# Performance work log

Measured on AMD Instinct MI355X. Metric: run time of the kernel, lower is better.

Reference implementation:

```python
import jax, jax.numpy as jnp
import numpy as np

N = 50000   # nodes
E = 512000  # edges
D = 64      # embedding_dim
L = 4       # num_layers
ATOM_DIMS = np.array([119, 5, 12, 12, 10, 6, 6, 2, 2])  # OGB atom feature vocab sizes
BOND_DIMS = np.array([5, 6, 2])                          # OGB bond feature vocab sizes


def _ln(x, g, b, eps=1e-5):
    m = x.mean(-1, keepdims=True)
    v = x.var(-1, keepdims=True)
    return (x - m) * jax.lax.rsqrt(v + eps) * g + b


def setup_inputs() -> dict:
    key = jax.random.key(0)
    ks = jax.random.split(key, 12)
    s = 0.05
    x = jax.random.randint(ks[0], (N, 9), 0, jnp.asarray(ATOM_DIMS)[None, :])
    edge_attr = jax.random.randint(ks[1], (E, 3), 0, jnp.asarray(BOND_DIMS)[None, :])
    edge_index = jax.random.randint(ks[2], (2, E), 0, N)
    # padded embedding tables: [n_feats, max_vocab, D]
    atom_emb = jax.random.normal(ks[3], (9, 119, D), jnp.float32) * s
    bond_emb = jax.random.normal(ks[4], (3, 6, D), jnp.float32) * s
    eps = jnp.zeros((L,), jnp.float32)  # GIN eps, init 0
    W1 = jax.random.normal(ks[5], (L, D, 2 * D), jnp.float32) * s
    b1 = jnp.zeros((L, 2 * D), jnp.float32)
    W2 = jax.random.normal(ks[6], (L, 2 * D, D), jnp.float32) * s
    b2 = jnp.zeros((L, D), jnp.float32)
    ln_g = jnp.ones((L, D), jnp.float32)
    ln_b = jnp.zeros((L, D), jnp.float32)
    Wu1 = jax.random.normal(ks[7], (L, 3 * D, 3 * D), jnp.float32) * s
    bu1 = jnp.zeros((L, 3 * D), jnp.float32)
    ug = jnp.ones((L, 3 * D), jnp.float32)
    ub = jnp.zeros((L, 3 * D), jnp.float32)
    Wu2 = jax.random.normal(ks[8], (L, 3 * D, D), jnp.float32) * s
    bu2 = jnp.zeros((L, D), jnp.float32)
    return dict(x=x, edge_attr=edge_attr, edge_index=edge_index,
                atom_emb=atom_emb, bond_emb=bond_emb, eps=eps,
                W1=W1, b1=b1, W2=W2, b2=b2, ln_g=ln_g, ln_b=ln_b,
                Wu1=Wu1, bu1=bu1, ug=ug, ub=ub, Wu2=Wu2, bu2=bu2)


def reference(x, edge_attr, edge_index, atom_emb, bond_emb, eps,
              W1, b1, W2, b2, ln_g, ln_b, Wu1, bu1, ug, ub, Wu2, bu2):
    # Atom/Bond encoders: sum of per-column categorical embeddings
    node = atom_emb[jnp.arange(9)[None, :], x].sum(axis=1)       # [N, D]
    edge = bond_emb[jnp.arange(3)[None, :], edge_attr].sum(axis=1)  # [E, D]
    src, dst = edge_index[0], edge_index[1]
    for l in range(L):
        # MyGINConv (GINE): aggregate relu(x_src + e) at dst, mlp((1+eps)x + agg)
        msg = jax.nn.relu(node[src] + edge)                      # [E, D]
        agg = jax.ops.segment_sum(msg, dst, num_segments=N)      # [N, D]
        h = (1.0 + eps[l]) * node + agg
        h = jax.nn.relu(h @ W1[l] + b1[l]) @ W2[l] + b2[l]       # conv MLP
        h = _ln(h, ln_g[l], ln_b[l])                             # batch_norms[l] (LayerNorm)
        node = jax.nn.relu(h) + node                             # dropout=identity (eval) + residual
        # SparseEdgeUpdateLayer (residual=True)
        cat = jnp.concatenate([node[src], node[dst], edge], axis=-1)  # [E, 3D]
        m = _ln(cat @ Wu1[l] + bu1[l], ug[l], ub[l])
        edge = jax.nn.relu(m) @ Wu2[l] + bu2[l] + edge
    return node, edge
```

## Files before the change

kernel.cpp:

```cpp
#include <hip/hip_runtime.h>
#include <hip/hip_bf16.h>


#define GIN_N 50000
#define GIN_E 512000

typedef __attribute__((ext_vector_type(8))) short short8;
typedef __attribute__((ext_vector_type(4))) float f32x4;
typedef unsigned short u16;

__device__ __forceinline__ u16 bf16r(float x) {
    unsigned u = __builtin_bit_cast(unsigned, x);
    u += 0x7fffu + ((u >> 16) & 1u);
    return (u16)(u >> 16);
}
__device__ __forceinline__ float bf16f(u16 h) {
    unsigned u = ((unsigned)h) << 16;
    return __builtin_bit_cast(float, u);
}

__global__ __launch_bounds__(256) void zero_f32(float* __restrict__ p, int n) {
    int i = blockIdx.x * 256 + threadIdx.x;
    if (i < n) p[i] = 0.f;
}
__global__ __launch_bounds__(256) void zero_i32(int* __restrict__ p, int n) {
    int i = blockIdx.x * 256 + threadIdx.x;
    if (i < n) p[i] = 0;
}

__global__ __launch_bounds__(256) void atom_encode(const int* __restrict__ x,
        const float* __restrict__ emb, float* __restrict__ node, int N) {
    int idx = blockIdx.x * 256 + threadIdx.x;
    int n = idx >> 6, lane = idx & 63;
    if (n >= N) return;
    float s = 0.f;
#pragma unroll
    for (int f = 0; f < 9; ++f) {
        int v = x[n * 9 + f];
        s += emb[(f * 119 + v) * 64 + lane];
    }
    node[(size_t)n * 64 + lane] = s;
}

__global__ __launch_bounds__(256) void csr_hist(const int* __restrict__ dst,
                                                int* __restrict__ deg, int E) {
    int e = blockIdx.x * 256 + threadIdx.x;
    if (e < E) atomicAdd(&deg[dst[e]], 1);
}
__global__ __launch_bounds__(256) void csr_scan(const int* __restrict__ deg,
                                                int* __restrict__ cursor, int N) {
    __shared__ int ps[256];
    const int t = threadIdx.x;
    const int chunk = (N + 255) / 256;
    const int base = t * chunk;
    int s = 0;
    for (int i = 0; i < chunk; ++i) {
        int idx = base + i;
        if (idx < N) s += deg[idx];
    }
    ps[t] = s;
    __syncthreads();
    for (int off = 1; off < 256; off <<= 1) {
        int v = (t >= off) ? ps[t - off] : 0;
        __syncthreads();
        ps[t] += v;
        __syncthreads();
    }
    int run = ps[t] - s;
    for (int i = 0; i < chunk; ++i) {
        int idx = base + i;
        if (idx < N) { cursor[idx] = run; run += deg[idx]; }
    }
}
__global__ __launch_bounds__(256) void csr_fill(const int* __restrict__ dst,
        int* __restrict__ cursor, int* __restrict__ perm, int E) {
    int e = blockIdx.x * 256 + threadIdx.x;
    if (e < E) {
        int d = dst[e];
        int pos = atomicAdd(&cursor[d], 1);
        perm[pos] = e;
    }
}
__global__ __launch_bounds__(256) void permute_ei(const int* __restrict__ src,
        const int* __restrict__ dst, const int* __restrict__ perm,
        int* __restrict__ srcS, int* __restrict__ dstS, int E) {
    int i = blockIdx.x * 256 + threadIdx.x;
    if (i < E) {
        int pe = perm[i];
        srcS[i] = src[pe];
        dstS[i] = dst[pe];
    }
}

__global__ __launch_bounds__(256) void bond_encode_scatter(
        const int* __restrict__ ea, const float* __restrict__ emb,
        u16* __restrict__ edgeB, const int* __restrict__ perm,
        const int* __restrict__ srcS, const int* __restrict__ dstS,
        const float* __restrict__ node, float* __restrict__ agg, int E) {
    int idx = blockIdx.x * 256 + threadIdx.x;
    int e = idx >> 6, lane = idx & 63;
    if (e >= E) return;
    int pe = perm[e];
    float s = 0.f;
#pragma unroll
    for (int f = 0; f < 3; ++f) {
        int v = ea[pe * 3 + f];
        s += emb[(f * 6 + v) * 64 + lane];
    }
    edgeB[(size_t)e * 64 + lane] = bf16r(s);
    int si = srcS[e], di = dstS[e];
    float msg = fmaxf(node[(size_t)si * 64 + lane] + s, 0.f);
    unsafeAtomicAdd(&agg[(size_t)di * 64 + lane], msg);
}

__global__ __launch_bounds__(256) void pack_b1(const float* __restrict__ W,
        u16* __restrict__ out, int K, int Nc, int F) {
    int tid = blockIdx.x * 256 + threadIdx.x;
    int lane = tid & 63;
    int frag = (tid >> 6) % F;
    int layer = tid / (F * 64);
    int tpr = Nc / 16;
    int ks = frag / tpr, tt = frag % tpr;
    int k0 = ks * 32 + ((lane >> 4) << 3);
    int col = tt * 16 + (lane & 15);
    const float* w = W + (size_t)layer * K * Nc;
    u16* o = out + ((size_t)layer * F + frag) * 512 + (size_t)lane * 8;
#pragma unroll
    for (int j = 0; j < 8; ++j) o[j] = bf16r(w[(size_t)(k0 + j) * Nc + col]);
}
__global__ __launch_bounds__(256) void pack_b2(const float* __restrict__ W,
        u16* __restrict__ out, int K, int Nc, int F) {
    int tid = blockIdx.x * 256 + threadIdx.x;
    int lane = tid & 63;
    int frag = (tid >> 6) % F;
    int layer = tid / (F * 64);
    int tpr = Nc / 16;
    int ks = frag / tpr, tt = frag % tpr;
    int k0 = ks * 32 + ((lane >> 4) << 3);
    int col = tt * 16 + (lane & 15);
    const float* w = W + (size_t)layer * K * Nc;
    u16* o = out + ((size_t)layer * F + frag) * 1024 + (size_t)lane * 8;
#pragma unroll
    for (int j = 0; j < 8; ++j) {
        float v = w[(size_t)(k0 + j) * Nc + col];
        u16 hi = bf16r(v);
        o[j] = hi;
        o[512 + j] = bf16r(v - bf16f(hi));
    }
}

__global__ __launch_bounds__(256, 2) void node_mlp(
        float* __restrict__ node, u16* __restrict__ nodeB,
        float* __restrict__ agg,
        const float* __restrict__ epsArr, int l,
        const u16* __restrict__ pw1, const u16* __restrict__ pw2,
        const float* __restrict__ b1, const float* __restrict__ b2,
        const float* __restrict__ lng, const float* __restrict__ lnb, int N) {
    __shared__ u16 xH[64][72], xL[64][72];
    __shared__ u16 hH[64][136], hL[64][136];
    __shared__ float pS[4][64], pS2[4][64], lnM[64], lnR[64];
    const int t = threadIdx.x, w = t >> 6, lane = t & 63;
    const int g = lane >> 4, c0 = lane & 15;
    const float epf = 1.f + epsArr[l];

#pragma unroll
    for (int i = 0; i < 16; ++i) {
        int r = w * 16 + i;
        int n = blockIdx.x * 64 + r;
        float x = 0.f;
        if (n < N) {
            size_t o = (size_t)n * 64 + lane;
            x = epf * node[o] + agg[o];
            agg[o] = 0.f;
        }
        u16 h = bf16r(x);
        xH[r][lane] = h;
        xL[r][lane] = bf16r(x - bf16f(h));
    }
    __syncthreads();

    f32x4 a1[4][2];
#pragma unroll
    for (int sp = 0; sp < 4; ++sp)
#pragma unroll
        for (int lt = 0; lt < 2; ++lt) a1[sp][lt] = (f32x4)0.f;
#pragma unroll
    for (int ks = 0; ks < 2; ++ks) {
        short8 aH[4], aL[4];
#pragma unroll
        for (int sp = 0; sp < 4; ++sp) {
            aH[sp] = *(const short8*)&xH[sp * 16 + c0][ks * 32 + g * 8];
            aL[sp] = *(const short8*)&xL[sp * 16 + c0][ks * 32 + g * 8];
        }
#pragma unroll
        for (int lt = 0; lt < 2; ++lt) {
            const u16* p = pw1 + (size_t)(ks * 8 + w * 2 + lt) * 1024 + (size_t)lane * 8;
            short8 bH = *(const short8*)p;
            short8 bL = *(const short8*)(p + 512);
#pragma unroll
            for (int sp = 0; sp < 4; ++sp) {
                a1[sp][lt] = __builtin_amdgcn_mfma_f32_16x16x32_bf16(aH[sp], bH, a1[sp][lt], 0, 0, 0);
                a1[sp][lt] = __builtin_amdgcn_mfma_f32_16x16x32_bf16(aH[sp], bL, a1[sp][lt], 0, 0, 0);
                a1[sp][lt] = __builtin_amdgcn_mfma_f32_16x16x32_bf16(aL[sp], bH, a1[sp][lt], 0, 0, 0);
            }
        }
    }
#pragma unroll
    for (int lt = 0; lt < 2; ++lt) {
        int col = w * 32 + lt * 16 + c0;
        float bias = b1[col];
#pragma unroll
        for (int sp = 0; sp < 4; ++sp)
#pragma unroll
            for (int rg = 0; rg < 4; ++rg) {
                int r = sp * 16 + g * 4 + rg;
                float v = fmaxf(a1[sp][lt][rg] + bias, 0.f);
                u16 h = bf16r(v);
                hH[r][col] = h;
                hL[r][col] = bf16r(v - bf16f(h));
            }
    }
    __syncthreads();

    f32x4 a2[4];
#pragma unroll
    for (int sp = 0; sp < 4; ++sp) a2[sp] = (f32x4)0.f;
#pragma unroll
    for (int ks = 0; ks < 4; ++ks) {
        const u16* p = pw2 + (size_t)(ks * 4 + w) * 1024 + (size_t)lane * 8;
        short8 bH = *(const short8*)p;
        short8 bL = *(const short8*)(p + 512);
#pragma unroll
        for (int sp = 0; sp < 4; ++sp) {
            short8 aH = *(const short8*)&hH[sp * 16 + c0][ks * 32 + g * 8];
            short8 aL = *(const short8*)&hL[sp * 16 + c0][ks * 32 + g * 8];
            a2[sp] = __builtin_amdgcn_mfma_f32_16x16x32_bf16(aH, bH, a2[sp], 0, 0, 0);
            a2[sp] = __builtin_amdgcn_mfma_f32_16x16x32_bf16(aH, bL, a2[sp], 0, 0, 0);
            a2[sp] = __builtin_amdgcn_mfma_f32_16x16x32_bf16(aL, bH, a2[sp], 0, 0, 0);
        }
    }
    float bias2 = b2[w * 16 + c0];
    float s1v[4][4], s2v[4][4];
#pragma unroll
    for (int sp = 0; sp < 4; ++sp)
#pragma unroll
        for (int rg = 0; rg < 4; ++rg) {
            float v = a2[sp][rg] + bias2;
            a2[sp][rg] = v;
            s1v[sp][rg] = v;
            s2v[sp][rg] = v * v;
        }
#pragma unroll
    for (int off = 1; off < 16; off <<= 1)
#pragma unroll
        for (int sp = 0; sp < 4; ++sp)
#pragma unroll
            for (int rg = 0; rg < 4; ++rg) {
                s1v[sp][rg] += __shfl_xor(s1v[sp][rg], off);
                s2v[sp][rg] += __shfl_xor(s2v[sp][rg], off);
            }
    if (c0 == 0) {
#pragma unroll
        for (int sp = 0; sp < 4; ++sp)
#pragma unroll
            for (int rg = 0; rg < 4; ++rg) {
                int r = sp * 16 + g * 4 + rg;
                pS[w][r] = s1v[sp][rg];
                pS2[w][r] = s2v[sp][rg];
            }
    }
    __syncthreads();
    if (t < 64) {
        float a = pS[0][t] + pS[1][t] + pS[2][t] + pS[3][t];
        float b = pS2[0][t] + pS2[1][t] + pS2[2][t] + pS2[3][t];
        float mean = a * (1.f / 64.f);
        float var = b * (1.f / 64.f) - mean * mean;
        lnM[t] = mean;
        lnR[t] = rsqrtf(var + 1e-5f);
    }
    __syncthreads();

    int col = w * 16 + c0;
    float gg = lng[col], bc = lnb[col];
#pragma unroll
    for (int sp = 0; sp < 4; ++sp)
#pragma unroll
        for (int rg = 0; rg < 4; ++rg) {
            int r = sp * 16 + g * 4 + rg;
            int n = blockIdx.x * 64 + r;
            if (n < N) {
                size_t o = (size_t)n * 64 + col;
                float y = (a2[sp][rg] - lnM[r]) * lnR[r] * gg + bc;
                float out = fmaxf(y, 0.f) + node[o];
                node[o] = out;
                nodeB[o] = bf16r(out);
            }
        }
}

template <bool SCATTER>
__global__ __launch_bounds__(256, 4) void edge_update_v7(
        const int* __restrict__ src, const int* __restrict__ dst,
        const int* __restrict__ perm,
        const float* __restrict__ node, const u16* __restrict__ nodeB,
        u16* __restrict__ edgeB, float* __restrict__ edgeF,
        float* __restrict__ agg,
        const u16* __restrict__ pb1, const u16* __restrict__ pb2,
        const float* __restrict__ bu1, const float* __restrict__ ug,
        const float* __restrict__ ub, const float* __restrict__ bu2) {
    __shared__ u16 cat[64][202];
    __shared__ u16 eold[64][66];
    __shared__ float pS[4][64], pS2[4][64];
    __shared__ float lnM[64], lnR[64];
    __shared__ int dstL[64], srcL[64];
    const int t = threadIdx.x, w = t >> 6, lane = t & 63;
    const int g = lane >> 4, c0 = lane & 15;
    const int tile = (blockIdx.x & 7) * (gridDim.x >> 3) + (blockIdx.x >> 3);
    const long eB = (long)tile * 64;

    if (t < 64) { dstL[t] = dst[eB + t]; srcL[t] = src[eB + t]; }
#pragma unroll
    for (int i = 0; i < 16; ++i) {
        int r = w * 16 + i;
        long ge = eB + r;
        int s = src[ge], d = dst[ge];
        cat[r][lane]       = nodeB[(size_t)s * 64 + lane];
        cat[r][64 + lane]  = nodeB[(size_t)d * 64 + lane];
        u16 ev = edgeB[(size_t)ge * 64 + lane];
        cat[r][128 + lane] = ev;
        eold[r][lane] = ev;
    }
    __syncthreads();

    f32x4 acc[4][3];
#pragma unroll
    for (int sp = 0; sp < 4; ++sp)
#pragma unroll
        for (int lt = 0; lt < 3; ++lt) acc[sp][lt] = (f32x4)0.f;
#pragma unroll
    for (int ks = 0; ks < 6; ++ks) {
        short8 a[4];
#pragma unroll
        for (int sp = 0; sp < 4; ++sp)
            a[sp] = *(const short8*)&cat[sp * 16 + c0][ks * 32 + g * 8];
#pragma unroll
        for (int lt = 0; lt < 3; ++lt) {
            const u16* p = pb1 + (size_t)(ks * 12 + w * 3 + lt) * 512 + (size_t)lane * 8;
            short8 b = *(const short8*)p;
#pragma unroll
            for (int sp = 0; sp < 4; ++sp)
                acc[sp][lt] = __builtin_amdgcn_mfma_f32_16x16x32_bf16(a[sp], b, acc[sp][lt], 0, 0, 0);
        }
    }

    float bs[3];
#pragma unroll
    for (int lt = 0; lt < 3; ++lt) bs[lt] = bu1[w * 48 + lt * 16 + c0];
    float s1v[4][4], s2v[4][4];
#pragma unroll
    for (int sp = 0; sp < 4; ++sp)
#pragma unroll
        for (int rg = 0; rg < 4; ++rg) { s1v[sp][rg] = 0.f; s2v[sp][rg] = 0.f; }
#pragma unroll
    for (int sp = 0; sp < 4; ++sp)
#pragma unroll
        for (int lt = 0; lt < 3; ++lt)
#pragma unroll
            for (int rg = 0; rg < 4; ++rg) {
                float v = acc[sp][lt][rg] + bs[lt];
                acc[sp][lt][rg] = v;
                s1v[sp][rg] += v;
                s2v[sp][rg] += v * v;
            }
#pragma unroll
    for (int off = 1; off < 16; off <<= 1)
#pragma unroll
        for (int sp = 0; sp < 4; ++sp)
#pragma unroll
            for (int rg = 0; rg < 4; ++rg) {
                s1v[sp][rg] += __shfl_xor(s1v[sp][rg], off);
                s2v[sp][rg] += __shfl_xor(s2v[sp][rg], off);
            }
    if (c0 == 0) {
#pragma unroll
        for (int sp = 0; sp < 4; ++sp)
#pragma unroll
            for (int rg = 0; rg < 4; ++rg) {
                int r = sp * 16 + g * 4 + rg;
                pS[w][r] = s1v[sp][rg];
                pS2[w][r] = s2v[sp][rg];
            }
    }
    __syncthreads();
    if (t < 64) {
        float a = pS[0][t] + pS[1][t] + pS[2][t] + pS[3][t];
        float b = pS2[0][t] + pS2[1][t] + pS2[2][t] + pS2[3][t];
        float mean = a * (1.f / 192.f);
        float var = b * (1.f / 192.f) - mean * mean;
        lnM[t] = mean;
        lnR[t] = rsqrtf(var + 1e-5f);
    }
    __syncthreads();

#pragma unroll
    for (int lt = 0; lt < 3; ++lt) {
        int col = w * 48 + lt * 16 + c0;
        float gg = ug[col], bb = ub[col];
#pragma unroll
        for (int sp = 0; sp < 4; ++sp)
#pragma unroll
            for (int rg = 0; rg < 4; ++rg) {
                int r = sp * 16 + g * 4 + rg;
                float v = (acc[sp][lt][rg] - lnM[r]) * lnR[r] * gg + bb;
                cat[r][col] = bf16r(fmaxf(v, 0.f));
            }
    }
    __syncthreads();

    f32x4 a2[4];
#pragma unroll
    for (int sp = 0; sp < 4; ++sp) a2[sp] = (f32x4)0.f;
#pragma unroll
    for (int ks = 0; ks < 6; ++ks) {
        const u16* p = pb2 + (size_t)(ks * 4 + w) * 512 + (size_t)lane * 8;
        short8 b = *(const short8*)p;
#pragma unroll
        for (int sp = 0; sp < 4; ++sp) {
            short8 a = *(const short8*)&cat[sp * 16 + c0][ks * 32 + g * 8];
            a2[sp] = __builtin_amdgcn_mfma_f32_16x16x32_bf16(a, b, a2[sp], 0, 0, 0);
        }
    }
    __syncthreads();

    float* msgF = (float*)&cat[0][0];
    const int col = w * 16 + c0;
    const float bb2 = bu2[col];
#pragma unroll
    for (int sp = 0; sp < 4; ++sp)
#pragma unroll
        for (int rg = 0; rg < 4; ++rg) {
            int r = sp * 16 + g * 4 + rg;
            long ge = eB + r;
            float eNew = a2[sp][rg] + bb2 + bf16f(eold[r][col]);
            if (SCATTER) {
                edgeB[(size_t)ge * 64 + col] = bf16r(eNew);
                float msg = fmaxf(node[(size_t)srcL[r] * 64 + col] + eNew, 0.f);
                msgF[r * 66 + col] = msg;
            } else {
                edgeF[(size_t)perm[ge] * 64 + col] = eNew;
            }
        }

    if (SCATTER) {
        __syncthreads();
        const int colR = t & 63;
        const int h = t >> 6;
        float accm = 0.f;
#pragma unroll 1
        for (int r = h * 16; r < h * 16 + 16; ++r) {
            accm += msgF[r * 66 + colR];
            bool flush = (r == h * 16 + 15) || (dstL[r + 1] != dstL[r]);
            if (flush) {
                unsafeAtomicAdd(&agg[(size_t)dstL[r] * 64 + colR], accm);
                accm = 0.f;
            }
        }
    }
}

extern "C" void kernel_launch(void* const* d_in, const int* in_sizes, int n_in,
                              void* d_out, int out_size, void* d_ws, size_t ws_size,
                              hipStream_t stream) {
    const int*   x         = (const int*)d_in[0];
    const int*   edge_attr = (const int*)d_in[1];
    const int*   edge_index= (const int*)d_in[2];
    const float* atom_emb  = (const float*)d_in[3];
    const float* bond_emb  = (const float*)d_in[4];
    const float* eps       = (const float*)d_in[5];
    const float* W1        = (const float*)d_in[6];
    const float* b1        = (const float*)d_in[7];
    const float* W2        = (const float*)d_in[8];
    const float* b2        = (const float*)d_in[9];
    const float* ln_g      = (const float*)d_in[10];
    const float* ln_b      = (const float*)d_in[11];
    const float* Wu1       = (const float*)d_in[12];
    const float* bu1       = (const float*)d_in[13];
    const float* ug        = (const float*)d_in[14];
    const float* ub        = (const float*)d_in[15];
    const float* Wu2       = (const float*)d_in[16];
    const float* bu2       = (const float*)d_in[17];

    const int N = GIN_N, E = GIN_E;
    const int* src = edge_index;
    const int* dst = edge_index + E;

    float* node  = (float*)d_out;
    float* edgeF = (float*)d_out + (size_t)N * 64;

    char* ws = (char*)d_ws;
    float* agg   = (float*)ws;  ws += (size_t)N * 64 * 4;
    u16*   nodeB = (u16*)ws;    ws += (size_t)N * 64 * 2;
    u16*   edgeB = (u16*)ws;    ws += (size_t)E * 64 * 2;
    int*   perm  = (int*)ws;    ws += (size_t)E * 4;
    int*   srcS  = (int*)ws;    ws += (size_t)E * 4;
    int*   dstS  = (int*)ws;    ws += (size_t)E * 4;
    int*   deg   = (int*)ws;    ws += (size_t)N * 4;
    int*   cursor= (int*)ws;    ws += (size_t)(N + 1) * 4;
    u16* pb1     = (u16*)ws;    ws += (size_t)4 * 72 * 512 * 2;
    u16* pb2     = (u16*)ws;    ws += (size_t)4 * 24 * 512 * 2;
    u16* pw1     = (u16*)ws;    ws += (size_t)4 * 16 * 1024 * 2;
    u16* pw2     = (u16*)ws;    ws += (size_t)4 * 16 * 1024 * 2;

    pack_b1<<<(4 * 72 * 64) / 256, 256, 0, stream>>>(Wu1, pb1, 192, 192, 72);
    pack_b1<<<(4 * 24 * 64) / 256, 256, 0, stream>>>(Wu2, pb2, 192, 64, 24);
    pack_b2<<<(4 * 16 * 64) / 256, 256, 0, stream>>>(W1, pw1, 64, 128, 16);
    pack_b2<<<(4 * 16 * 64) / 256, 256, 0, stream>>>(W2, pw2, 128, 64, 16);

    zero_i32<<<(N + 255) / 256, 256, 0, stream>>>(deg, N);
    csr_hist<<<E / 256, 256, 0, stream>>>(dst, deg, E);
    csr_scan<<<1, 256, 0, stream>>>(deg, cursor, N);
    csr_fill<<<E / 256, 256, 0, stream>>>(dst, cursor, perm, E);
    permute_ei<<<E / 256, 256, 0, stream>>>(src, dst, perm, srcS, dstS, E);

    atom_encode<<<(N * 64 + 255) / 256, 256, 0, stream>>>(x, atom_emb, node, N);
    zero_f32<<<(N * 64) / 256, 256, 0, stream>>>(agg, N * 64);
    bond_encode_scatter<<<(E * 64) / 256, 256, 0, stream>>>(edge_attr, bond_emb,
        edgeB, perm, srcS, dstS, node, agg, E);

    const int nodeBlocks = (N + 63) / 64;
    for (int l = 0; l < 4; ++l) {
        node_mlp<<<nodeBlocks, 256, 0, stream>>>(node, nodeB, agg, eps, l,
            pw1 + (size_t)l * 16 * 1024, pw2 + (size_t)l * 16 * 1024,
            b1 + (size_t)l * 128, b2 + (size_t)l * 64,
            ln_g + (size_t)l * 64, ln_b + (size_t)l * 64, N);
        if (l < 3)
            edge_update_v7<true><<<E / 64, 256, 0, stream>>>(srcS, dstS, perm,
                node, nodeB, edgeB, edgeF, agg,
                pb1 + (size_t)l * 72 * 512, pb2 + (size_t)l * 24 * 512,
                bu1 + (size_t)l * 192,
                ug + (size_t)l * 192, ub + (size_t)l * 192,
                bu2 + (size_t)l * 64);
        else
            edge_update_v7<false><<<E / 64, 256, 0, stream>>>(srcS, dstS, perm,
                node, nodeB, edgeB, edgeF, agg,
                pb1 + (size_t)l * 72 * 512, pb2 + (size_t)l * 24 * 512,
                bu1 + (size_t)l * 192,
                ug + (size_t)l * 192, ub + (size_t)l * 192,
                bu2 + (size_t)l * 64);
    }
}
```

Baseline: 1.016 ms.

## Segment-reduce bond scatter, vectorize edge tile loads, drop eold LDS, widen scan

The initial bond-encode scatter now stages messages for a 64-edge tile in shared memory. It then does a segmented reduction over dst-sorted edges before the atomics, which cuts the number of atomic adds. The edge update kernel loads the edge tile with 8-byte vector loads, keeps the old edge values in registers instead of a separate LDS array, and raises the occupancy hint to 5 blocks per CU. The CSR scan uses 1024 threads. Together these aim to reduce atomic traffic and LDS use, with some added register pressure.

Result: slower. 1.243 ms (+22.3%).

```diff
diff --git a/kernel.cpp b/kernel.cpp
--- a/kernel.cpp
+++ b/kernel.cpp
@@ -6,6 +6,7 @@
 #define GIN_E 512000
 
 typedef __attribute__((ext_vector_type(8))) short short8;
+typedef __attribute__((ext_vector_type(4))) short short4v;
 typedef __attribute__((ext_vector_type(4))) float f32x4;
 typedef unsigned short u16;
 
@@ -47,11 +48,11 @@
     int e = blockIdx.x * 256 + threadIdx.x;
     if (e < E) atomicAdd(&deg[dst[e]], 1);
 }
-__global__ __launch_bounds__(256) void csr_scan(const int* __restrict__ deg,
-                                                int* __restrict__ cursor, int N) {
-    __shared__ int ps[256];
+__global__ __launch_bounds__(1024) void csr_scan(const int* __restrict__ deg,
+                                                 int* __restrict__ cursor, int N) {
+    __shared__ int ps[1024];
     const int t = threadIdx.x;
-    const int chunk = (N + 255) / 256;
+    const int chunk = (N + 1023) / 1024;
     const int base = t * chunk;
     int s = 0;
     for (int i = 0; i < chunk; ++i) {
@@ -60,7 +61,7 @@
     }
     ps[t] = s;
     __syncthreads();
-    for (int off = 1; off < 256; off <<= 1) {
+    for (int off = 1; off < 1024; off <<= 1) {
         int v = (t >= off) ? ps[t - off] : 0;
         __syncthreads();
         ps[t] += v;
@@ -92,25 +93,45 @@
     }
 }
 
-__global__ __launch_bounds__(256) void bond_encode_scatter(
+__global__ __launch_bounds__(256) void bond_encode_seg(
         const int* __restrict__ ea, const float* __restrict__ emb,
         u16* __restrict__ edgeB, const int* __restrict__ perm,
         const int* __restrict__ srcS, const int* __restrict__ dstS,
-        const float* __restrict__ node, float* __restrict__ agg, int E) {
-    int idx = blockIdx.x * 256 + threadIdx.x;
-    int e = idx >> 6, lane = idx & 63;
-    if (e >= E) return;
-    int pe = perm[e];
-    float s = 0.f;
-#pragma unroll
-    for (int f = 0; f < 3; ++f) {
-        int v = ea[pe * 3 + f];
-        s += emb[(f * 6 + v) * 64 + lane];
-    }
-    edgeB[(size_t)e * 64 + lane] = bf16r(s);
-    int si = srcS[e], di = dstS[e];
-    float msg = fmaxf(node[(size_t)si * 64 + lane] + s, 0.f);
-    unsafeAtomicAdd(&agg[(size_t)di * 64 + lane], msg);
+        const float* __restrict__ node, float* __restrict__ agg) {
+    __shared__ float msgF[64][66];
+    __shared__ int dstL[64];
+    const int t = threadIdx.x, w = t >> 6, lane = t & 63;
+    const int tile = (blockIdx.x & 7) * (gridDim.x >> 3) + (blockIdx.x >> 3);
+    const long eB = (long)tile * 64;
+
+    if (t < 64) dstL[t] = dstS[eB + t];
+#pragma unroll 1
+    for (int i = 0; i < 16; ++i) {
+        int r = w * 16 + i;
+        long e = eB + r;
+        int pe = perm[e];
+        float s = 0.f;
+#pragma unroll
+        for (int f = 0; f < 3; ++f) {
+            int v = ea[pe * 3 + f];
+            s += emb[(f * 6 + v) * 64 + lane];
+        }
+        edgeB[(size_t)e * 64 + lane] = bf16r(s);
+        int si = srcS[e];
+        msgF[r][lane] = fmaxf(node[(size_t)si * 64 + lane] + s, 0.f);
+    }
+    __syncthreads();
+    const int colR = t & 63;
+    const int h = t >> 6;
+    float acc = 0.f;
+#pragma unroll 1
+    for (int r = h * 16; r < h * 16 + 16; ++r) {
+        acc += msgF[r][colR];
+        if (r == h * 16 + 15 || dstL[r + 1] != dstL[r]) {
+            unsafeAtomicAdd(&agg[(size_t)dstL[r] * 64 + colR], acc);
+            acc = 0.f;
+        }
+    }
 }
 
 __global__ __launch_bounds__(256) void pack_b1(const float* __restrict__ W,
@@ -299,7 +320,7 @@
 }
 
 template <bool SCATTER>
-__global__ __launch_bounds__(256, 4) void edge_update_v7(
+__global__ __launch_bounds__(256, 5) void edge_update_v8(
         const int* __restrict__ src, const int* __restrict__ dst,
         const int* __restrict__ perm,
         const float* __restrict__ node, const u16* __restrict__ nodeB,
@@ -309,7 +330,6 @@
         const float* __restrict__ bu1, const float* __restrict__ ug,
         const float* __restrict__ ub, const float* __restrict__ bu2) {
     __shared__ u16 cat[64][202];
-    __shared__ u16 eold[64][66];
     __shared__ float pS[4][64], pS2[4][64];
     __shared__ float lnM[64], lnR[64];
     __shared__ int dstL[64], srcL[64];
@@ -324,13 +344,26 @@
         int r = w * 16 + i;
         long ge = eB + r;
         int s = src[ge], d = dst[ge];
-        cat[r][lane]       = nodeB[(size_t)s * 64 + lane];
-        cat[r][64 + lane]  = nodeB[(size_t)d * 64 + lane];
-        u16 ev = edgeB[(size_t)ge * 64 + lane];
-        cat[r][128 + lane] = ev;
-        eold[r][lane] = ev;
-    }
-    __syncthreads();
+        cat[r][lane]      = nodeB[(size_t)s * 64 + lane];
+        cat[r][64 + lane] = nodeB[(size_t)d * 64 + lane];
+    }
+    {
+        const u16* eTile = edgeB + (size_t)eB * 64;
+#pragma unroll
+        for (int q = 0; q < 4; ++q) {
+            int gi = t + q * 256;
+            int r = gi >> 4, c4 = (gi & 15) * 4;
+            *(short4v*)&cat[r][128 + c4] = *(const short4v*)(eTile + gi * 4);
+        }
+    }
+    __syncthreads();
+
+    u16 eold16[16];
+#pragma unroll
+    for (int sp = 0; sp < 4; ++sp)
+#pragma unroll
+        for (int rg = 0; rg < 4; ++rg)
+            eold16[sp * 4 + rg] = cat[sp * 16 + g * 4 + rg][128 + w * 16 + c0];
 
     f32x4 acc[4][3];
 #pragma unroll
@@ -441,7 +474,7 @@
         for (int rg = 0; rg < 4; ++rg) {
             int r = sp * 16 + g * 4 + rg;
             long ge = eB + r;
-            float eNew = a2[sp][rg] + bb2 + bf16f(eold[r][col]);
+            float eNew = a2[sp][rg] + bb2 + bf16f(eold16[sp * 4 + rg]);
             if (SCATTER) {
                 edgeB[(size_t)ge * 64 + col] = bf16r(eNew);
                 float msg = fmaxf(node[(size_t)srcL[r] * 64 + col] + eNew, 0.f);
@@ -459,8 +492,7 @@
 #pragma unroll 1
         for (int r = h * 16; r < h * 16 + 16; ++r) {
             accm += msgF[r * 66 + colR];
-            bool flush = (r == h * 16 + 15) || (dstL[r + 1] != dstL[r]);
-            if (flush) {
+            if (r == h * 16 + 15 || dstL[r + 1] != dstL[r]) {
                 unsafeAtomicAdd(&agg[(size_t)dstL[r] * 64 + colR], accm);
                 accm = 0.f;
             }
@@ -518,14 +550,14 @@
 
     zero_i32<<<(N + 255) / 256, 256, 0, stream>>>(deg, N);
     csr_hist<<<E / 256, 256, 0, stream>>>(dst, deg, E);
-    csr_scan<<<1, 256, 0, stream>>>(deg, cursor, N);
+    csr_scan<<<1, 1024, 0, stream>>>(deg, cursor, N);
     csr_fill<<<E / 256, 256, 0, stream>>>(dst, cursor, perm, E);
     permute_ei<<<E / 256, 256, 0, stream>>>(src, dst, perm, srcS, dstS, E);
 
     atom_encode<<<(N * 64 + 255) / 256, 256, 0, stream>>>(x, atom_emb, node, N);
     zero_f32<<<(N * 64) / 256, 256, 0, stream>>>(agg, N * 64);
-    bond_encode_scatter<<<(E * 64) / 256, 256, 0, stream>>>(edge_attr, bond_emb,
-        edgeB, perm, srcS, dstS, node, agg, E);
+    bond_encode_seg<<<E / 64, 256, 0, stream>>>(edge_attr, bond_emb,
+        edgeB, perm, srcS, dstS, node, agg);
 
     const int nodeBlocks = (N + 63) / 64;
     for (int l = 0; l < 4; ++l) {
@@ -534,14 +566,14 @@
             b1 + (size_t)l * 128, b2 + (size_t)l * 64,
             ln_g + (size_t)l * 64, ln_b + (size_t)l * 64, N);
         if (l < 3)
-            edge_update_v7<true><<<E / 64, 256, 0, stream>>>(srcS, dstS, perm,
+            edge_update_v8<true><<<E / 64, 256, 0, stream>>>(srcS, dstS, perm,
                 node, nodeB, edgeB, edgeF, agg,
                 pb1 + (size_t)l * 72 * 512, pb2 + (size_t)l * 24 * 512,
                 bu1 + (size_t)l * 192,
                 ug + (size_t)l * 192, ub + (size_t)l * 192,
                 bu2 + (size_t)l * 64);
         else
-            edge_update_v7<false><<<E / 64, 256, 0, stream>>>(srcS, dstS, perm,
+            edge_update_v8<false><<<E / 64, 256, 0, stream>>>(srcS, dstS, perm,
                 node, nodeB, edgeB, edgeF, agg,
                 pb1 + (size_t)l * 72 * 512, pb2 + (size_t)l * 24 * 512,
                 bu1 + (size_t)l * 192,
```
